# Kernel optimization log

Hardware: AMD Instinct MI355X
Metric: run time of the kernel (lower is better)

The kernel has to match this reference:

```python
import jax, jax.numpy as jnp
import numpy as np

B, L, E = 8, 2048, 4096
TOKEN_DIM, EDGE_DIM, HIDDEN = 768, 256, 128


def setup_inputs() -> dict:
    key = jax.random.key(0)
    k1, k2, k3, k4, k5 = jax.random.split(key, 5)
    token_embedding = jax.random.normal(k1, (B, L, TOKEN_DIM), dtype=jnp.float32)
    edge_embedding = jax.random.normal(k2, (B, E, EDGE_DIM), dtype=jnp.float32)
    # fc: Linear(token_dim+edge_dim -> hidden, bias=False); stored as [in, out]
    W_fc = jax.random.normal(k3, (TOKEN_DIM + EDGE_DIM, HIDDEN), dtype=jnp.float32) * 0.02
    # attn_fc: Linear(2*hidden -> 1); weight flattened to [2*hidden], plus scalar bias
    a_attn = jax.random.normal(k4, (2 * HIDDEN,), dtype=jnp.float32) * 0.02
    b_attn = jax.random.normal(k5, (1,), dtype=jnp.float32) * 0.02
    return {"token_embedding": token_embedding, "edge_embedding": edge_embedding,
            "W_fc": W_fc, "a_attn": a_attn, "b_attn": b_attn}


def reference(token_embedding, edge_embedding, W_fc, a_attn, b_attn):
    # avg edge embedding, broadcast over sequence
    avg_edge = edge_embedding.mean(axis=1, keepdims=True)          # [B, 1, De]
    avg_edge = jnp.broadcast_to(avg_edge, (token_embedding.shape[0],
                                           token_embedding.shape[1],
                                           avg_edge.shape[-1]))     # [B, L, De]
    combined = jnp.concatenate([token_embedding, avg_edge], axis=-1)  # [B, L, Dt+De]
    h = jnp.einsum('bld,dh->blh', combined, W_fc)                   # [B, L, H]

    # Additive attention decomposition: a^T [h_j || h_i] = a1.h_j + a2.h_i
    # (original builds concat([h_repeat_row (=h_j), h_repeat_col (=h_i)]))
    H = h.shape[-1]
    a1, a2 = a_attn[:H], a_attn[H:]
    s_j = jnp.einsum('blh,h->bl', h, a1)                            # score contrib from h_j
    s_i = jnp.einsum('blh,h->bl', h, a2)                            # score contrib from h_i
    scores = s_i[:, :, None] + s_j[:, None, :] + b_attn[0]          # [B, L, L], scores[b,i,j]
    attn = jax.nn.softmax(scores, axis=-1)                          # softmax over j
    h_prime = jnp.einsum('bij,bjh->bih', attn, h)                   # [B, L, H]
    return h_prime
```

## Files before the change

kernel.cpp:

```cpp
#include <hip/hip_runtime.h>

constexpr int Bn  = 8;
constexpr int Ln  = 2048;
constexpr int En  = 4096;
constexpr int TDn = 768;
constexpr int EDn = 256;
constexpr int Hn  = 128;

constexpr int OFF_V1   = 0;
constexpr int OFF_TREC = 1024;
constexpr int TRECF    = 772;
constexpr int OFF_EREC = OFF_TREC + 512 * TRECF;

__global__ __launch_bounds__(256)
void K_0(const float* __restrict__ W, const float* __restrict__ a,
         float* __restrict__ ws)
{
    const int tid = threadIdx.x, wv = tid >> 6, lane = tid & 63;
    int d = blockIdx.x * 4 + wv;
    float acc = W[d * Hn + lane]      * a[lane]
              + W[d * Hn + 64 + lane] * a[64 + lane];
    #pragma unroll
    for (int off = 32; off > 0; off >>= 1)
        acc += __shfl_down(acc, off, 64);
    if (lane == 0) ws[OFF_V1 + d] = acc;
}

__global__ __launch_bounds__(256)
void K_1(const float* __restrict__ token, const float* __restrict__ edge,
         float* __restrict__ ws)
{
    const int tid = threadIdx.x, wv = tid >> 6, lane = tid & 63;
    const int bi = blockIdx.x;
    __shared__ __align__(16) float4 smf[4 * 192];
    __shared__ float sm_den[4];

    if (bi < 512) {
        const int b = bi >> 6, chunk = bi & 63;
        const size_t row0 = (size_t)b * Ln + chunk * 32 + wv * 8;

        const float4* v1_4 = (const float4*)(ws + OFF_V1);
        float4 u0 = v1_4[lane], u1 = v1_4[64 + lane], u2 = v1_4[128 + lane];

        const float4* t4 = (const float4*)token + row0 * (TDn / 4);
        float4 a0 = {0,0,0,0}, a1 = {0,0,0,0}, a2 = {0,0,0,0};
        float esum = 0.f;

        float4 p0 = t4[lane], p1 = t4[64 + lane], p2 = t4[128 + lane];
        #pragma unroll
        for (int i = 0; i < 8; ++i) {
            float4 n0 = p0, n1 = p1, n2 = p2;
            if (i < 7) {
                const float4* nt = t4 + (size_t)(i + 1) * 192;
                n0 = nt[lane]; n1 = nt[64 + lane]; n2 = nt[128 + lane];
            }
            float d = p0.x*u0.x + p0.y*u0.y + p0.z*u0.z + p0.w*u0.w
                    + p1.x*u1.x + p1.y*u1.y + p1.z*u1.z + p1.w*u1.w
                    + p2.x*u2.x + p2.y*u2.y + p2.z*u2.z + p2.w*u2.w;
            #pragma unroll
            for (int off = 32; off > 0; off >>= 1)
                d += __shfl_xor(d, off, 64);
            float e = expf(d);
            esum += e;
            a0.x += e*p0.x; a0.y += e*p0.y; a0.z += e*p0.z; a0.w += e*p0.w;
            a1.x += e*p1.x; a1.y += e*p1.y; a1.z += e*p1.z; a1.w += e*p1.w;
            a2.x += e*p2.x; a2.y += e*p2.y; a2.z += e*p2.z; a2.w += e*p2.w;
            p0 = n0; p1 = n1; p2 = n2;
        }

        smf[wv * 192 + lane]       = a0;
        smf[wv * 192 + 64 + lane]  = a1;
        smf[wv * 192 + 128 + lane] = a2;
        if (lane == 0) sm_den[wv] = esum;
        __syncthreads();

        float* rec = ws + OFF_TREC + (size_t)bi * TRECF;
        if (tid < 192) {
            float4 r  = smf[tid];
            float4 q1 = smf[192 + tid], q2 = smf[384 + tid], q3 = smf[576 + tid];
            r.x += q1.x + q2.x + q3.x;  r.y += q1.y + q2.y + q3.y;
            r.z += q1.z + q2.z + q3.z;  r.w += q1.w + q2.w + q3.w;
            ((float4*)(rec + 4))[tid] = r;
        }
        if (tid == 0)
            rec[0] = sm_den[0] + sm_den[1] + sm_den[2] + sm_den[3];
    } else {
        const int eb = bi - 512;
        const int b = eb >> 6, chunk = eb & 63;
        const size_t row0 = (size_t)b * En + chunk * 64 + wv * 16;
        const float4* e4 = (const float4*)edge + row0 * (EDn / 4) + lane;
        float4 acc = {0,0,0,0};
        #pragma unroll
        for (int i = 0; i < 16; ++i) {
            float4 v = e4[(size_t)i * (EDn / 4)];
            acc.x += v.x; acc.y += v.y; acc.z += v.z; acc.w += v.w;
        }
        smf[wv * 64 + lane] = acc;
        __syncthreads();
        if (tid < 64) {
            float4 r0 = smf[tid],       r1 = smf[64 + tid],
                   r2 = smf[128 + tid], r3 = smf[192 + tid];
            float4 s = {r0.x + r1.x + r2.x + r3.x, r0.y + r1.y + r2.y + r3.y,
                        r0.z + r1.z + r2.z + r3.z, r0.w + r1.w + r2.w + r3.w};
            ((float4*)(ws + OFF_EREC))[(size_t)eb * 64 + tid] = s;
        }
    }
}

__global__ __launch_bounds__(256)
void K_2(const float* __restrict__ W, const float* __restrict__ ws,
         float4* __restrict__ out)
{
    __shared__ __align__(16) float s_c[1024];
    __shared__ __align__(16) float4 smp[256];
    __shared__ __align__(16) float4 s_row[32];
    __shared__ float s_den;
    const int tid = threadIdx.x;
    const int b = blockIdx.x >> 3, slice = blockIdx.x & 7;

    if (tid < 64) {
        float dv = ws[OFF_TREC + (size_t)(b * 64 + tid) * TRECF];
        #pragma unroll
        for (int off = 32; off > 0; off >>= 1)
            dv += __shfl_xor(dv, off, 64);
        if (tid == 0) s_den = dv;
    }

    float4 acc = {0,0,0,0};
    if (tid < 192) {
        const float4* rb = (const float4*)(ws + OFF_TREC)
                         + (size_t)(b * 64) * (TRECF / 4) + 1 + tid;
        #pragma unroll 8
        for (int k = 0; k < 64; ++k) {
            float4 v = rb[(size_t)k * (TRECF / 4)];
            acc.x += v.x; acc.y += v.y; acc.z += v.z; acc.w += v.w;
        }
    } else {
        const float4* rb = (const float4*)(ws + OFF_EREC)
                         + (size_t)(b * 64) * (EDn / 4) + (tid - 192);
        #pragma unroll 8
        for (int k = 0; k < 64; ++k) {
            float4 v = rb[(size_t)k * (EDn / 4)];
            acc.x += v.x; acc.y += v.y; acc.z += v.z; acc.w += v.w;
        }
    }
    __syncthreads();

    float scale = (tid < 192) ? (1.0f / s_den) : (1.0f / En);
    float4 c = {acc.x * scale, acc.y * scale, acc.z * scale, acc.w * scale};
    ((float4*)s_c)[tid] = c;
    __syncthreads();

    const int hq = tid & 31, dg = tid >> 5;
    const float4* W4 = (const float4*)W;
    const float* cp = s_c + dg * 128;
    float4 m = {0,0,0,0};
    #pragma unroll 8
    for (int i = 0; i < 128; ++i) {
        float cv = cp[i];
        float4 w = W4[(size_t)(dg * 128 + i) * (Hn / 4) + hq];
        m.x += cv * w.x; m.y += cv * w.y; m.z += cv * w.z; m.w += cv * w.w;
    }
    smp[tid] = m;
    __syncthreads();
    if (tid < 32) {
        float4 r = smp[tid];
        #pragma unroll
        for (int g = 1; g < 8; ++g) {
            float4 v = smp[g * 32 + tid];
            r.x += v.x; r.y += v.y; r.z += v.z; r.w += v.w;
        }
        s_row[tid] = r;
    }
    __syncthreads();

    float4* ob = out + ((size_t)b * Ln + slice * 256) * (Hn / 4);
    #pragma unroll
    for (int k = 0; k < 32; ++k) {
        int f = k * 256 + tid;
        ob[f] = s_row[f & 31];
    }
}

extern "C" void kernel_launch(void* const* d_in, const int* in_sizes, int n_in,
                              void* d_out, int out_size, void* d_ws, size_t ws_size,
                              hipStream_t stream) {
    const float* token = (const float*)d_in[0];
    const float* edge  = (const float*)d_in[1];
    const float* W     = (const float*)d_in[2];
    const float* a     = (const float*)d_in[3];
    float* ws   = (float*)d_ws;
    float4* out = (float4*)d_out;

    K_0<<<192,  256, 0, stream>>>(W, a, ws);
    K_1<<<1024, 256, 0, stream>>>(token, edge, ws);
    K_2<<<64,   256, 0, stream>>>(W, ws, out);
}
```

Baseline: 128.2 us.

## Fuse W·a projection into token pass and split output write across more blocks

Removes the separate K_0 launch by having each token block recompute the 768-entry projection of W_fc onto a1 into shared memory before its softmax-weighted token reduction. This drops one kernel launch and the workspace round trip, at the cost of redundant W reads (768x128 floats per block, 512 blocks) and two extra block barriers. Separately, K_2 now uses 128 blocks each writing 128 rows instead of 64 blocks writing 256 rows, to spread the output broadcast store over more CUs.

Result: slower. 147.6 us (+15.2%).

```diff
diff --git a/kernel.cpp b/kernel.cpp
--- a/kernel.cpp
+++ b/kernel.cpp
@@ -7,43 +7,48 @@
 constexpr int EDn = 256;
 constexpr int Hn  = 128;
 
-constexpr int OFF_V1   = 0;
-constexpr int OFF_TREC = 1024;
+constexpr int OFF_TREC = 0;
 constexpr int TRECF    = 772;
-constexpr int OFF_EREC = OFF_TREC + 512 * TRECF;
-
-__global__ __launch_bounds__(256)
-void K_0(const float* __restrict__ W, const float* __restrict__ a,
-         float* __restrict__ ws)
-{
-    const int tid = threadIdx.x, wv = tid >> 6, lane = tid & 63;
-    int d = blockIdx.x * 4 + wv;
-    float acc = W[d * Hn + lane]      * a[lane]
-              + W[d * Hn + 64 + lane] * a[64 + lane];
-    #pragma unroll
-    for (int off = 32; off > 0; off >>= 1)
-        acc += __shfl_down(acc, off, 64);
-    if (lane == 0) ws[OFF_V1 + d] = acc;
-}
+constexpr int OFF_EREC = 512 * TRECF;
 
 __global__ __launch_bounds__(256)
 void K_1(const float* __restrict__ token, const float* __restrict__ edge,
+         const float* __restrict__ W, const float* __restrict__ a,
          float* __restrict__ ws)
 {
     const int tid = threadIdx.x, wv = tid >> 6, lane = tid & 63;
     const int bi = blockIdx.x;
     __shared__ __align__(16) float4 smf[4 * 192];
+    __shared__ __align__(16) float sv1[TDn];
+    __shared__ __align__(16) float sa[128];
     __shared__ float sm_den[4];
 
     if (bi < 512) {
         const int b = bi >> 6, chunk = bi & 63;
         const size_t row0 = (size_t)b * Ln + chunk * 32 + wv * 8;
 
-        const float4* v1_4 = (const float4*)(ws + OFF_V1);
+        if (tid < 32) ((float4*)sa)[tid] = ((const float4*)a)[tid];
+        __syncthreads();
+        const float4* av = (const float4*)sa;
+        #pragma unroll
+        for (int r = 0; r < 3; ++r) {
+            int d = tid + r * 256;
+            const float4* w4 = (const float4*)(W + (size_t)d * Hn);
+            float acc = 0.f;
+            #pragma unroll 8
+            for (int j = 0; j < 32; ++j) {
+                float4 w = w4[j], aa = av[j];
+                acc += w.x * aa.x + w.y * aa.y + w.z * aa.z + w.w * aa.w;
+            }
+            sv1[d] = acc;
+        }
+        __syncthreads();
+
+        const float4* v1_4 = (const float4*)sv1;
         float4 u0 = v1_4[lane], u1 = v1_4[64 + lane], u2 = v1_4[128 + lane];
 
         const float4* t4 = (const float4*)token + row0 * (TDn / 4);
-        float4 a0 = {0,0,0,0}, a1 = {0,0,0,0}, a2 = {0,0,0,0};
+        float4 a0 = {0,0,0,0}, a1v = {0,0,0,0}, a2 = {0,0,0,0};
         float esum = 0.f;
 
         float4 p0 = t4[lane], p1 = t4[64 + lane], p2 = t4[128 + lane];
@@ -63,13 +68,13 @@
             float e = expf(d);
             esum += e;
             a0.x += e*p0.x; a0.y += e*p0.y; a0.z += e*p0.z; a0.w += e*p0.w;
-            a1.x += e*p1.x; a1.y += e*p1.y; a1.z += e*p1.z; a1.w += e*p1.w;
+            a1v.x += e*p1.x; a1v.y += e*p1.y; a1v.z += e*p1.z; a1v.w += e*p1.w;
             a2.x += e*p2.x; a2.y += e*p2.y; a2.z += e*p2.z; a2.w += e*p2.w;
             p0 = n0; p1 = n1; p2 = n2;
         }
 
         smf[wv * 192 + lane]       = a0;
-        smf[wv * 192 + 64 + lane]  = a1;
+        smf[wv * 192 + 64 + lane]  = a1v;
         smf[wv * 192 + 128 + lane] = a2;
         if (lane == 0) sm_den[wv] = esum;
         __syncthreads();
@@ -116,7 +121,7 @@
     __shared__ __align__(16) float4 s_row[32];
     __shared__ float s_den;
     const int tid = threadIdx.x;
-    const int b = blockIdx.x >> 3, slice = blockIdx.x & 7;
+    const int b = blockIdx.x >> 4, slice = blockIdx.x & 15;
 
     if (tid < 64) {
         float dv = ws[OFF_TREC + (size_t)(b * 64 + tid) * TRECF];
@@ -174,9 +179,9 @@
     }
     __syncthreads();
 
-    float4* ob = out + ((size_t)b * Ln + slice * 256) * (Hn / 4);
+    float4* ob = out + ((size_t)b * Ln + slice * 128) * (Hn / 4);
     #pragma unroll
-    for (int k = 0; k < 32; ++k) {
+    for (int k = 0; k < 16; ++k) {
         int f = k * 256 + tid;
         ob[f] = s_row[f & 31];
     }
@@ -192,7 +197,6 @@
     float* ws   = (float*)d_ws;
     float4* out = (float4*)d_out;
 
-    K_0<<<192,  256, 0, stream>>>(W, a, ws);
-    K_1<<<1024, 256, 0, stream>>>(token, edge, ws);
-    K_2<<<64,   256, 0, stream>>>(W, ws, out);
+    K_1<<<1024, 256, 0, stream>>>(token, edge, W, a, ws);
+    K_2<<<128,  256, 0, stream>>>(W, ws, out);
 }
```
